# Kernel optimization log

Hardware: AMD Instinct MI355X
Metric: run time of the kernel (lower is better)

Reference implementation:

```python
import jax, jax.numpy as jnp
import numpy as np

N_HEADS = 4
N_NODES = 10000
EMB = 128
N_BATCH = 4096
N_NEAREST = 8
N_SENTINELS = 8


def setup_inputs() -> dict:
    key = jax.random.key(0)
    k1, k2, k3, k4 = jax.random.split(key, 4)
    embeds = jax.random.normal(k1, (N_HEADS, N_NODES, EMB), jnp.float32)
    field = jax.random.uniform(k3, (N_HEADS, N_NODES, EMB), dtype=jnp.float32)
    uncertainty = jnp.ones((1, 1, 1), jnp.float32) * 5.0
    adj = (jax.random.uniform(k4, (N_NODES, N_NODES)) < 0.001).astype(jnp.float32)
    batch_edges = jax.random.randint(k2, (2, N_BATCH), 0, N_NODES)
    return {"embeds": embeds, "field": field, "uncertainty": uncertainty,
            "adj": adj, "batch_edges": batch_edges}


def _knn_samples(embeds, nodes, k):
    # embeds: (h, n, d); nodes: (b,) -> indices of k nearest neighbors, excluding self.
    # Squared L2 distance is monotone in L2 norm, so top-k order matches the
    # original's .norm(dim=3).topk(..., largest=False).
    x = embeds[:, nodes]                                  # (h, b, d)
    x2 = jnp.sum(x * x, axis=-1)[:, :, None]              # (h, b, 1)
    y2 = jnp.sum(embeds * embeds, axis=-1)[:, None, :]    # (h, 1, n)
    d2 = x2 + y2 - 2.0 * jnp.einsum('hbd,hnd->hbn', x, embeds)  # (h, b, n)
    _, idx = jax.lax.top_k(-d2, k + 1)                    # nearest first
    return jax.lax.stop_gradient(idx[:, :, 1:])           # drop self -> (h, b, k)


def reference(embeds, field, uncertainty, adj, batch_edges):
    src, dst = batch_edges[0], batch_edges[1]
    h_idx = jnp.arange(N_HEADS)[:, None, None]

    def build(nodes, nodes_logits, adj_gather):
        samples = _knn_samples(embeds, nodes, N_NEAREST)                 # (h,b,k)
        diff = embeds[:, nodes][:, :, None, :] - embeds[h_idx, samples]  # (h,b,k,d)
        label = uncertainty * (adj_gather(samples) * 2.0 - 1.0)          # (h,b,k)
        g = field[:, nodes_logits]                                        # (h,b,d)
        logits = jnp.einsum('hbkd,hbd->hbk', diff, g) + label
        return logits, diff

    src_logits, src_diff = build(src, dst, lambda s: adj[s, dst[None, :, None]])
    tgt_logits, tgt_diff = build(dst, src, lambda s: adj[src[None, :, None], s])

    logits = jnp.concatenate([src_logits, tgt_logits], axis=2)           # (h,b,2k)
    dist = jnp.linalg.norm(jnp.concatenate([src_diff, tgt_diff], axis=2), axis=3)

    h, b = logits.shape[0], logits.shape[1]
    logits = jnp.concatenate(
        [logits, jnp.zeros((h, b, N_SENTINELS), logits.dtype)], axis=2)
    dist = jnp.concatenate(
        [dist, jnp.ones((h, b, N_SENTINELS), dist.dtype)], axis=2)

    # softmin: softmax(1 - dist)-weighted sum of logits, then mean over heads
    softmin = jnp.sum(logits * jax.nn.softmax(1.0 - dist, axis=2), axis=2)  # (h,b)
    return jax.nn.sigmoid(softmin.mean(axis=0)).reshape(-1)                 # (b,)
```

## Files before the change

### kernel.cpp

```cpp
#include <hip/hip_runtime.h>
#include <math.h>
#include <stdint.h>

#define N_HEADS 4
#define N_NODES 10000
#define NPAD 10112
#define NPG (NPAD / 32)
#define EMB 128
#define N_BATCH 4096
#define NQ (2 * N_BATCH)
#define K 8
#define TQ 64
#define TN 128
#define NTILES (NPAD / TN)
#define PH 2
#define CAP 41
#define WIN 0.5f

typedef __attribute__((ext_vector_type(8))) __bf16 bf16x8;
typedef __attribute__((ext_vector_type(8))) unsigned short ushortx8;
typedef __attribute__((ext_vector_type(16))) float floatx16;

__device__ __forceinline__ unsigned short f2bf(float x) {
  unsigned u = __float_as_uint(x);
  u += 0x7fff + ((u >> 16) & 1);
  return (unsigned short)(u >> 16);
}
__device__ __forceinline__ uint32_t bfup(float f) {
  uint32_t u = __float_as_uint(f);
  return (f >= 0.f) ? ((u + 0xFFFFu) >> 16) : (u >> 16);
}

__device__ __forceinline__ void insert8(float* bs, int* bi, float s, int node) {
  if (s < bs[K - 1]) {
    #pragma unroll
    for (int k2 = K - 1; k2 >= 0; --k2) {
      if (!(s < bs[k2])) break;
      if (k2 < K - 1) { bs[k2 + 1] = bs[k2]; bi[k2 + 1] = bi[k2]; }
      bs[k2] = s; bi[k2] = node;
    }
  }
}

__device__ __forceinline__ size_t pchunk(int g, int c, int lm) {
  return (size_t)g * 4096 + (size_t)(c >> 1) * 512 + (size_t)(c & 1) * 256 + lm * 8;
}

__global__ __launch_bounds__(256) void prep_kernel(
    const float* __restrict__ E, unsigned short* __restrict__ EhiP,
    float* __restrict__ y2g) {
  __shared__ float s_p[8][33];
  const int h = blockIdx.y, g = blockIdx.x;
  const int lm = threadIdx.x & 31, c8 = threadIdx.x >> 5;
  const int n = g * 32 + lm;
  float x[16];
  #pragma unroll
  for (int j = 0; j < 16; ++j) x[j] = 0.f;
  if (n < N_NODES) {
    const float* src = E + (size_t)(h * N_NODES + n) * EMB + c8 * 16;
    #pragma unroll
    for (int j = 0; j < 4; ++j) {
      float4 v = *(const float4*)(src + j * 4);
      x[j * 4 + 0] = v.x; x[j * 4 + 1] = v.y; x[j * 4 + 2] = v.z; x[j * 4 + 3] = v.w;
    }
  }
  float part = 0.f;
  ushortx8 hi[2];
  #pragma unroll
  for (int j = 0; j < 16; ++j) {
    part += x[j] * x[j];
    hi[j >> 3][j & 7] = f2bf(x[j]);
  }
  size_t base = (size_t)h * NPG * 4096;
  #pragma unroll
  for (int lh = 0; lh < 2; ++lh)
    *(ushortx8*)&EhiP[base + pchunk(g, c8 * 2 + lh, lm)] = hi[lh];
  s_p[c8][lm] = part;
  __syncthreads();
  if (threadIdx.x < 32) {
    int nn = g * 32 + threadIdx.x;
    float s = 0.f;
    #pragma unroll
    for (int j = 0; j < 8; ++j) s += s_p[j][threadIdx.x];
    y2g[h * NPAD + nn] = (nn < N_NODES) ? s : 1e30f;
  }
}

__global__ __launch_bounds__(256)
__attribute__((amdgpu_waves_per_eu(2, 2)))
void knn_kernel(
    const unsigned short* __restrict__ EhiP, const float* __restrict__ y2g,
    const float* __restrict__ Ef, const int* __restrict__ be,
    int* __restrict__ samples) {
  __shared__ __align__(16) float s_x[TQ * TN];
  __shared__ float s_t8S[TQ * 9];
  __shared__ int   s_t8I[TQ * 9];
  __shared__ float s_lsS[TQ * CAP];
  __shared__ int   s_lsI[TQ * CAP];
  __shared__ float s_thr[TQ];
  __shared__ int   s_cnt[TQ];

  const int id = blockIdx.x;
  const int h = (id & 7) >> 1;
  const int qt = ((id >> 3) << 1) | (id & 1);
  const int tid = threadIdx.x;
  const int lane = tid & 63;
  const int w1 = tid >> 6;
  const int lm = lane & 31, lh = lane >> 5;
  const unsigned short* EhiH = EhiP + (size_t)h * NPG * 4096;
  const float* y2H = y2g + h * NPAD;
  const float* EH = Ef + (size_t)h * N_NODES * EMB;

  bf16x8 a0[8], a1[8];
  {
    int q0 = be[qt * TQ + lm];
    int q1 = be[qt * TQ + 32 + lm];
    int g0 = q0 >> 5, l0 = q0 & 31;
    int g1 = q1 >> 5, l1 = q1 & 31;
    #pragma unroll
    for (int ks = 0; ks < 8; ++ks) {
      a0[ks] = *(const bf16x8*)&EhiH[pchunk(g0, ks * 2 + lh, l0)];
      a1[ks] = *(const bf16x8*)&EhiH[pchunk(g1, ks * 2 + lh, l1)];
    }
  }

  const int qsel = tid >> 2;
  const int csel = tid & 3;
  const int myq = be[qt * TQ + qsel];
  float bs[K]; int bi[K];
  #pragma unroll
  for (int k2 = 0; k2 < K; ++k2) { bs[k2] = 1e30f; bi[k2] = 0x7fffffff; }
  if (tid < TQ) s_cnt[tid] = 0;

  const int bnode = 32 * w1 + lm;
  const unsigned short* bhp = EhiH + (size_t)w1 * 4096 + lane * 8;

  #pragma unroll 1
  for (int t = 0; t < PH; ++t) {
    const size_t goff = (size_t)t * 16384;
    float ny = y2H[t * TN + bnode];
    floatx16 acc0 = {0.f, 0.f, 0.f, 0.f, 0.f, 0.f, 0.f, 0.f,
                     0.f, 0.f, 0.f, 0.f, 0.f, 0.f, 0.f, 0.f};
    floatx16 acc1 = acc0;
    #pragma unroll
    for (int ks = 0; ks < 8; ++ks) {
      bf16x8 vbh = *(const bf16x8*)(bhp + goff + ks * 512);
      acc0 = __builtin_amdgcn_mfma_f32_32x32x16_bf16(a0[ks], vbh, acc0, 0, 0, 0);
      acc1 = __builtin_amdgcn_mfma_f32_32x32x16_bf16(a1[ks], vbh, acc1, 0, 0, 0);
    }
    #pragma unroll
    for (int r = 0; r < 16; ++r) {
      int row = (r & 3) + 8 * (r >> 2) + 4 * lh;
      s_x[row * TN + bnode] = fmaf(-2.f, acc0[r], ny);
      s_x[(row + 32) * TN + bnode] = fmaf(-2.f, acc1[r], ny);
    }
    __syncthreads();
    int nbp = t * TN;
    #pragma unroll
    for (int s = 0; s < 32; ++s) {
      int j = csel * 32 + ((s + qsel) & 31);
      float sc = s_x[qsel * TN + j];
      int node = nbp + j;
      if (node != myq) insert8(bs, bi, sc, node);
    }
    __syncthreads();
  }

  {
    float* scrS = (float*)s_x;
    int*   scrI = (int*)s_x + TQ * 32;
    #pragma unroll
    for (int k2 = 0; k2 < K; ++k2) {
      scrS[tid * 8 + k2] = bs[k2]; scrI[tid * 8 + k2] = bi[k2];
    }
    __syncthreads();
    if (tid < TQ) {
      int q = tid;
      float ts[K]; int ti[K];
      #pragma unroll
      for (int k2 = 0; k2 < K; ++k2) { ts[k2] = 1e30f; ti[k2] = 0x7fffffff; }
      for (int kk = 0; kk < 32; ++kk) {
        int e = (kk + q) & 31;
        insert8(ts, ti, scrS[q * 32 + e], scrI[q * 32 + e]);
      }
      float thr = ts[K - 1], win = thr + WIN;
      int nc = 0;
      for (int kk = 0; kk < 32; ++kk) {
        int e = (kk + q) & 31;
        float sv = scrS[q * 32 + e]; int iv = scrI[q * 32 + e];
        if (sv <= win && nc < CAP) {
          bool dup = false;
          #pragma unroll
          for (int j = 0; j < K; ++j) dup = dup || (ti[j] == iv);
          if (!dup) { s_lsS[q * CAP + nc] = sv; s_lsI[q * CAP + nc] = iv; ++nc; }
        }
      }
      s_cnt[q] = nc;
      s_thr[q] = win;
      #pragma unroll
      for (int k2 = 0; k2 < K; ++k2) { s_t8S[q * 9 + k2] = ts[k2]; s_t8I[q * 9 + k2] = ti[k2]; }
    }
    __syncthreads();
  }

  uint32_t thrp0[8], thrp1[8];
  #pragma unroll
  for (int j = 0; j < 8; ++j) {
    int r0 = 2 * j, r1 = 2 * j + 1;
    int w0 = (r0 & 3) + 8 * (r0 >> 2) + 4 * lh;
    int w1r = (r1 & 3) + 8 * (r1 >> 2) + 4 * lh;
    thrp0[j] = bfup(s_thr[w0]) | (bfup(s_thr[w1r]) << 16);
    thrp1[j] = bfup(s_thr[w0 + 32]) | (bfup(s_thr[w1r + 32]) << 16);
  }

#define PREFETCH_T(VB, NY, TT)                                               \
  do {                                                                       \
    const size_t goff_ = (size_t)(TT) * 16384;                               \
    NY = y2H[(TT) * TN + bnode];                                             \
    _Pragma("unroll")                                                        \
    for (int ks = 0; ks < 8; ++ks)                                           \
      VB[ks] = *(const bf16x8*)(bhp + goff_ + ks * 512);                     \
  } while (0)

#define COMPUTE_T(VB, NY, TT)                                                \
  do {                                                                       \
    floatx16 acc0 = {0.f, 0.f, 0.f, 0.f, 0.f, 0.f, 0.f, 0.f,                 \
                     0.f, 0.f, 0.f, 0.f, 0.f, 0.f, 0.f, 0.f};                \
    floatx16 acc1 = acc0;                                                    \
    _Pragma("unroll")                                                        \
    for (int ks = 0; ks < 8; ++ks) {                                         \
      acc0 = __builtin_amdgcn_mfma_f32_32x32x16_bf16(a0[ks], VB[ks], acc0, 0, 0, 0); \
      acc1 = __builtin_amdgcn_mfma_f32_32x32x16_bf16(a1[ks], VB[ks], acc1, 0, 0, 0); \
    }                                                                        \
    const int node_ = (TT) * TN + bnode;                                     \
    _Pragma("unroll")                                                        \
    for (int r = 0; r < 16; ++r) {                                           \
      float sc = fmaf(-2.f, acc0[r], NY);                                    \
      float th = (r & 1) ? __uint_as_float(thrp0[r >> 1] & 0xFFFF0000u)      \
                         : __uint_as_float(thrp0[r >> 1] << 16);             \
      if (sc < th) {                                                         \
        int q_ = (r & 3) + 8 * (r >> 2) + 4 * lh;                            \
        int p_ = atomicAdd(&s_cnt[q_], 1);                                   \
        if (p_ < CAP) { s_lsS[q_ * CAP + p_] = sc; s_lsI[q_ * CAP + p_] = node_; } \
      }                                                                      \
    }                                                                        \
    _Pragma("unroll")                                                        \
    for (int r = 0; r < 16; ++r) {                                           \
      float sc = fmaf(-2.f, acc1[r], NY);                                    \
      float th = (r & 1) ? __uint_as_float(thrp1[r >> 1] & 0xFFFF0000u)      \
                         : __uint_as_float(thrp1[r >> 1] << 16);             \
      if (sc < th) {                                                         \
        int q_ = 32 + (r & 3) + 8 * (r >> 2) + 4 * lh;                       \
        int p_ = atomicAdd(&s_cnt[q_], 1);                                   \
        if (p_ < CAP) { s_lsS[q_ * CAP + p_] = sc; s_lsI[q_ * CAP + p_] = node_; } \
      }                                                                      \
    }                                                                        \
  } while (0)

  bf16x8 vbA[8], vbB[8];
  float nyA = 0.f, nyB = 0.f;
  PREFETCH_T(vbA, nyA, PH);

  #pragma unroll 1
  for (int t = PH; t + 2 < NTILES; t += 2) {
    if (t == 4 || t == 8 || t == 16 || t == 32) {
      __syncthreads();
      if (tid < TQ) {
        int q = tid;
        int myqm = be[qt * TQ + q];
        float ts[K]; int ti[K];
        #pragma unroll
        for (int k2 = 0; k2 < K; ++k2) { ts[k2] = s_t8S[q * 9 + k2]; ti[k2] = s_t8I[q * 9 + k2]; }
        int cnt = s_cnt[q]; if (cnt > CAP) cnt = CAP;
        for (int p = 0; p < cnt; ++p) {
          int iv = s_lsI[q * CAP + p];
          if (iv != myqm) insert8(ts, ti, s_lsS[q * CAP + p], iv);
        }
        float thr = ts[K - 1], win = thr + WIN;
        int nc = 0;
        for (int p = 0; p < cnt; ++p) {
          float sv = s_lsS[q * CAP + p]; int iv = s_lsI[q * CAP + p];
          if (sv <= win && iv != myqm) {
            bool dup = false;
            #pragma unroll
            for (int j = 0; j < K; ++j) dup = dup || (ti[j] == iv);
            if (!dup && nc < CAP) { s_lsS[q * CAP + nc] = sv; s_lsI[q * CAP + nc] = iv; ++nc; }
          }
        }
        #pragma unroll
        for (int k2 = 0; k2 < K; ++k2) {
          float sv = s_t8S[q * 9 + k2]; int iv = s_t8I[q * 9 + k2];
          if (sv <= win && iv != myqm && nc < CAP) {
            bool dup = false;
            #pragma unroll
            for (int j = 0; j < K; ++j) dup = dup || (ti[j] == iv);
            if (!dup) { s_lsS[q * CAP + nc] = sv; s_lsI[q * CAP + nc] = iv; ++nc; }
          }
        }
        s_cnt[q] = nc;
        s_thr[q] = win;
        #pragma unroll
        for (int k2 = 0; k2 < K; ++k2) { s_t8S[q * 9 + k2] = ts[k2]; s_t8I[q * 9 + k2] = ti[k2]; }
      }
      __syncthreads();
      #pragma unroll
      for (int j = 0; j < 8; ++j) {
        int r0 = 2 * j, r1 = 2 * j + 1;
        int w0 = (r0 & 3) + 8 * (r0 >> 2) + 4 * lh;
        int w1r = (r1 & 3) + 8 * (r1 >> 2) + 4 * lh;
        thrp0[j] = bfup(s_thr[w0]) | (bfup(s_thr[w1r]) << 16);
        thrp1[j] = bfup(s_thr[w0 + 32]) | (bfup(s_thr[w1r + 32]) << 16);
      }
    }

    PREFETCH_T(vbB, nyB, t + 1);
    __builtin_amdgcn_sched_barrier(0);
    COMPUTE_T(vbA, nyA, t);
    PREFETCH_T(vbA, nyA, t + 2);
    __builtin_amdgcn_sched_barrier(0);
    COMPUTE_T(vbB, nyB, t + 1);
  }
  COMPUTE_T(vbA, nyA, NTILES - 1);
#undef PREFETCH_T
#undef COMPUTE_T

  __syncthreads();
  {
    int q = tid >> 2, k4 = tid & 3;
    int qn = be[qt * TQ + q];
    const float4* Eq = (const float4*)(EH + (size_t)qn * EMB);
    #pragma unroll
    for (int kk = 0; kk < 2; ++kk) {
      int k = k4 + kk * 4;
      int iv = s_t8I[q * 9 + k];
      if (iv < N_NODES) {
        const float4* En = (const float4*)(EH + (size_t)iv * EMB);
        float d0 = 0.f, d1 = 0.f, d2 = 0.f, d3 = 0.f;
        #pragma unroll
        for (int d = 0; d < 32; ++d) {
          float4 a = Eq[d], b = En[d];
          d0 += a.x * b.x; d1 += a.y * b.y; d2 += a.z * b.z; d3 += a.w * b.w;
        }
        s_t8S[q * 9 + k] = y2H[iv] - 2.f * ((d0 + d1) + (d2 + d3));
      }
    }
    int cnt = s_cnt[q]; if (cnt > CAP) cnt = CAP;
    for (int p = k4; p < cnt; p += 4) {
      int jv = s_lsI[q * CAP + p];
      if (jv < N_NODES && jv != qn) {
        const float4* En = (const float4*)(EH + (size_t)jv * EMB);
        float d0 = 0.f, d1 = 0.f, d2 = 0.f, d3 = 0.f;
        #pragma unroll
        for (int d = 0; d < 32; ++d) {
          float4 a = Eq[d], b = En[d];
          d0 += a.x * b.x; d1 += a.y * b.y; d2 += a.z * b.z; d3 += a.w * b.w;
        }
        s_lsS[q * CAP + p] = y2H[jv] - 2.f * ((d0 + d1) + (d2 + d3));
      }
    }
  }
  __syncthreads();
  if (tid < TQ) {
    int q = tid;
    int myqm = be[qt * TQ + q];
    float ts[K]; int ti[K];
    #pragma unroll
    for (int k2 = 0; k2 < K; ++k2) { ts[k2] = 1e30f; ti[k2] = 0x7fffffff; }
    #pragma unroll
    for (int k2 = 0; k2 < K; ++k2)
      insert8(ts, ti, s_t8S[q * 9 + k2], s_t8I[q * 9 + k2]);
    int cnt = s_cnt[q]; if (cnt > CAP) cnt = CAP;
    for (int p = 0; p < cnt; ++p) {
      int iv = s_lsI[q * CAP + p];
      if (iv != myqm) insert8(ts, ti, s_lsS[q * CAP + p], iv);
    }
    size_t base = ((size_t)h * NQ + qt * TQ + q) * K;
    #pragma unroll
    for (int k2 = 0; k2 < K; ++k2) samples[base + k2] = ti[k2];
  }
}

__global__ __launch_bounds__(256) void predict_kernel(
    const float* __restrict__ E, const float* __restrict__ F,
    const float* __restrict__ unc, const float* __restrict__ adj,
    const int* __restrict__ be, const int* __restrict__ samples,
    float* __restrict__ out) {
  int b = blockIdx.x;
  int h = threadIdx.x >> 6;
  int lane = threadIdx.x & 63;
  __shared__ float smv[N_HEADS];

  int srcb = be[b];
  int dstb = be[N_BATCH + b];
  const float* Eh = E + (size_t)h * N_NODES * EMB;
  const float* Fh = F + (size_t)h * N_NODES * EMB;
  float2 es = *(const float2*)(Eh + (size_t)srcb * EMB + 2 * lane);
  float2 ed = *(const float2*)(Eh + (size_t)dstb * EMB + 2 * lane);
  float2 fs = *(const float2*)(Fh + (size_t)srcb * EMB + 2 * lane);
  float2 fd = *(const float2*)(Fh + (size_t)dstb * EMB + 2 * lane);
  float u = unc[0];

  float logit[16], dist[16];
  #pragma unroll
  for (int j = 0; j < 16; ++j) {
    bool isrc = (j < 8);
    int qrow = isrc ? b : (N_BATCH + b);
    int s = samples[((size_t)h * NQ + qrow) * K + (j & 7)];
    float2 ev = *(const float2*)(Eh + (size_t)s * EMB + 2 * lane);
    float2 bb = isrc ? es : ed;
    float2 g = isrc ? fd : fs;
    float dx = bb.x - ev.x, dy = bb.y - ev.y;
    float dot = dx * g.x + dy * g.y;
    float nrm = dx * dx + dy * dy;
    #pragma unroll
    for (int o = 32; o > 0; o >>= 1) {
      dot += __shfl_xor(dot, o);
      nrm += __shfl_xor(nrm, o);
    }
    float a = isrc ? adj[(size_t)s * N_NODES + dstb]
                   : adj[(size_t)srcb * N_NODES + s];
    logit[j] = dot + u * (2.0f * a - 1.0f);
    dist[j] = sqrtf(nrm);
  }

  float m = 0.0f;
  #pragma unroll
  for (int j = 0; j < 16; ++j) m = fmaxf(m, 1.0f - dist[j]);
  float Z = 8.0f * expf(-m);
  float num = 0.0f;
  #pragma unroll
  for (int j = 0; j < 16; ++j) {
    float e = expf(1.0f - dist[j] - m);
    Z += e;
    num += logit[j] * e;
  }
  if (lane == 0) smv[h] = num / Z;
  __syncthreads();
  if (threadIdx.x == 0) {
    float t = 0.25f * (smv[0] + smv[1] + smv[2] + smv[3]);
    out[b] = 1.0f / (1.0f + expf(-t));
  }
}

extern "C" void kernel_launch(void* const* d_in, const int* in_sizes, int n_in,
                              void* d_out, int out_size, void* d_ws,
                              size_t ws_size, hipStream_t stream) {
  const float* E = (const float*)d_in[0];
  const float* F = (const float*)d_in[1];
  const float* U = (const float*)d_in[2];
  const float* A = (const float*)d_in[3];
  const int* be = (const int*)d_in[4];
  float* out = (float*)d_out;

  char* w = (char*)d_ws;
  unsigned short* EhiP = (unsigned short*)(w);
  float* y2g = (float*)(w + 10354688);
  int* samples = (int*)(w + 10516736);

  prep_kernel<<<dim3(NPG, N_HEADS), 256, 0, stream>>>(E, EhiP, y2g);
  knn_kernel<<<dim3((NQ / TQ) * N_HEADS), 256, 0, stream>>>(EhiP, y2g, E, be, samples);
  predict_kernel<<<dim3(N_BATCH), 256, 0, stream>>>(E, F, U, A, be, samples, out);
}
```

Baseline: 775.9 us.

## Compute neighbor diff norms and field dots in knn epilogue; slim predict kernel

After selecting the top-8 neighbors, the knn kernel now computes, per query and neighbor, the squared diff norm and its dot product with the partner field row. It writes these as a float2 buffer. The predict kernel then only loads these scalars and the adjacency entries, and does one lane per (head, neighbor), with four batch items per block and shuffle reductions. This drops the redundant embedding gathers and the cross-wave shared-memory reduction from predict, at the cost of per-thread serial 128-dim loops in the knn epilogue that read rows uncoalesced.

Result: slower. 807.8 us (+4.1%).

```diff
diff --git a/kernel.cpp b/kernel.cpp
--- a/kernel.cpp
+++ b/kernel.cpp
@@ -90,8 +90,9 @@
 __attribute__((amdgpu_waves_per_eu(2, 2)))
 void knn_kernel(
     const unsigned short* __restrict__ EhiP, const float* __restrict__ y2g,
-    const float* __restrict__ Ef, const int* __restrict__ be,
-    int* __restrict__ samples) {
+    const float* __restrict__ Ef, const float* __restrict__ Ff,
+    const int* __restrict__ be, int* __restrict__ samples,
+    float2* __restrict__ ld) {
   __shared__ __align__(16) float s_x[TQ * TN];
   __shared__ float s_t8S[TQ * 9];
   __shared__ int   s_t8I[TQ * 9];
@@ -110,6 +111,7 @@
   const unsigned short* EhiH = EhiP + (size_t)h * NPG * 4096;
   const float* y2H = y2g + h * NPAD;
   const float* EH = Ef + (size_t)h * N_NODES * EMB;
+  const float* FH = Ff + (size_t)h * N_NODES * EMB;
 
   bf16x8 a0[8], a1[8];
   {
@@ -376,70 +378,78 @@
     }
     size_t base = ((size_t)h * NQ + qt * TQ + q) * K;
     #pragma unroll
-    for (int k2 = 0; k2 < K; ++k2) samples[base + k2] = ti[k2];
+    for (int k2 = 0; k2 < K; ++k2) {
+      samples[base + k2] = ti[k2];
+      s_t8I[q * 9 + k2] = ti[k2];
+    }
+  }
+  __syncthreads();
+
+  {
+    int q = tid >> 2, k4 = tid & 3;
+    int Q = qt * TQ + q;
+    int qn = be[Q];
+    int pn = be[Q ^ N_BATCH];
+    const float4* Eq = (const float4*)(EH + (size_t)qn * EMB);
+    const float4* G  = (const float4*)(FH + (size_t)pn * EMB);
+    #pragma unroll
+    for (int kk = 0; kk < 2; ++kk) {
+      int k = k4 + kk * 4;
+      int s = s_t8I[q * 9 + k];
+      const float4* En = (const float4*)(EH + (size_t)s * EMB);
+      float n0 = 0.f, n1 = 0.f, n2 = 0.f, n3 = 0.f;
+      float g0 = 0.f, g1 = 0.f, g2 = 0.f, g3 = 0.f;
+      #pragma unroll
+      for (int d = 0; d < 32; ++d) {
+        float4 a = Eq[d], b = En[d], c = G[d];
+        float dx = a.x - b.x, dy = a.y - b.y, dz = a.z - b.z, dw = a.w - b.w;
+        n0 += dx * dx; n1 += dy * dy; n2 += dz * dz; n3 += dw * dw;
+        g0 += dx * c.x; g1 += dy * c.y; g2 += dz * c.z; g3 += dw * c.w;
+      }
+      float nrm = (n0 + n1) + (n2 + n3);
+      float dot2 = (g0 + g1) + (g2 + g3);
+      ld[((size_t)h * NQ + Q) * K + k] = make_float2(dot2, sqrtf(nrm));
+    }
   }
 }
 
 __global__ __launch_bounds__(256) void predict_kernel(
-    const float* __restrict__ E, const float* __restrict__ F,
     const float* __restrict__ unc, const float* __restrict__ adj,
     const int* __restrict__ be, const int* __restrict__ samples,
-    float* __restrict__ out) {
-  int b = blockIdx.x;
-  int h = threadIdx.x >> 6;
+    const float2* __restrict__ ld, float* __restrict__ out) {
+  int b = blockIdx.x * 4 + (threadIdx.x >> 6);
   int lane = threadIdx.x & 63;
-  __shared__ float smv[N_HEADS];
-
+  int h = lane >> 4, j = lane & 15;
   int srcb = be[b];
   int dstb = be[N_BATCH + b];
-  const float* Eh = E + (size_t)h * N_NODES * EMB;
-  const float* Fh = F + (size_t)h * N_NODES * EMB;
-  float2 es = *(const float2*)(Eh + (size_t)srcb * EMB + 2 * lane);
-  float2 ed = *(const float2*)(Eh + (size_t)dstb * EMB + 2 * lane);
-  float2 fs = *(const float2*)(Fh + (size_t)srcb * EMB + 2 * lane);
-  float2 fd = *(const float2*)(Fh + (size_t)dstb * EMB + 2 * lane);
+  bool isrc = (j < 8);
+  int qrow = isrc ? b : (N_BATCH + b);
+  int k = j & 7;
+  size_t qi = ((size_t)h * NQ + qrow) * K + k;
+  int s = samples[qi];
+  float2 dd = ld[qi];
   float u = unc[0];
-
-  float logit[16], dist[16];
-  #pragma unroll
-  for (int j = 0; j < 16; ++j) {
-    bool isrc = (j < 8);
-    int qrow = isrc ? b : (N_BATCH + b);
-    int s = samples[((size_t)h * NQ + qrow) * K + (j & 7)];
-    float2 ev = *(const float2*)(Eh + (size_t)s * EMB + 2 * lane);
-    float2 bb = isrc ? es : ed;
-    float2 g = isrc ? fd : fs;
-    float dx = bb.x - ev.x, dy = bb.y - ev.y;
-    float dot = dx * g.x + dy * g.y;
-    float nrm = dx * dx + dy * dy;
-    #pragma unroll
-    for (int o = 32; o > 0; o >>= 1) {
-      dot += __shfl_xor(dot, o);
-      nrm += __shfl_xor(nrm, o);
-    }
-    float a = isrc ? adj[(size_t)s * N_NODES + dstb]
-                   : adj[(size_t)srcb * N_NODES + s];
-    logit[j] = dot + u * (2.0f * a - 1.0f);
-    dist[j] = sqrtf(nrm);
-  }
-
-  float m = 0.0f;
-  #pragma unroll
-  for (int j = 0; j < 16; ++j) m = fmaxf(m, 1.0f - dist[j]);
-  float Z = 8.0f * expf(-m);
-  float num = 0.0f;
-  #pragma unroll
-  for (int j = 0; j < 16; ++j) {
-    float e = expf(1.0f - dist[j] - m);
-    Z += e;
-    num += logit[j] * e;
-  }
-  if (lane == 0) smv[h] = num / Z;
-  __syncthreads();
-  if (threadIdx.x == 0) {
-    float t = 0.25f * (smv[0] + smv[1] + smv[2] + smv[3]);
-    out[b] = 1.0f / (1.0f + expf(-t));
-  }
+  float a = isrc ? adj[(size_t)s * N_NODES + dstb]
+                 : adj[(size_t)srcb * N_NODES + s];
+  float logit = dd.x + u * (2.0f * a - 1.0f);
+  float dist = dd.y;
+
+  float m = fmaxf(0.0f, 1.0f - dist);
+  #pragma unroll
+  for (int o = 8; o > 0; o >>= 1) m = fmaxf(m, __shfl_xor(m, o));
+  float e = expf(1.0f - dist - m);
+  float Z = e, num = logit * e;
+  #pragma unroll
+  for (int o = 8; o > 0; o >>= 1) {
+    Z += __shfl_xor(Z, o);
+    num += __shfl_xor(num, o);
+  }
+  Z += 8.0f * expf(-m);
+  float smv = num / Z;
+  float t = smv;
+  t += __shfl_xor(t, 16);
+  t += __shfl_xor(t, 32);
+  if (lane == 0) out[b] = 1.0f / (1.0f + expf(-0.25f * t));
 }
 
 extern "C" void kernel_launch(void* const* d_in, const int* in_sizes, int n_in,
@@ -456,8 +466,9 @@
   unsigned short* EhiP = (unsigned short*)(w);
   float* y2g = (float*)(w + 10354688);
   int* samples = (int*)(w + 10516736);
+  float2* ld = (float2*)(w + 11565312);
 
   prep_kernel<<<dim3(NPG, N_HEADS), 256, 0, stream>>>(E, EhiP, y2g);
-  knn_kernel<<<dim3((NQ / TQ) * N_HEADS), 256, 0, stream>>>(EhiP, y2g, E, be, samples);
-  predict_kernel<<<dim3(N_BATCH), 256, 0, stream>>>(E, F, U, A, be, samples, out);
-}
+  knn_kernel<<<dim3((NQ / TQ) * N_HEADS), 256, 0, stream>>>(EhiP, y2g, E, F, be, samples, ld);
+  predict_kernel<<<dim3(N_BATCH / 4), 256, 0, stream>>>(U, A, be, samples, ld, out);
+}
```
